# Kernel tuning notes

Measured on AMD Instinct MI355X. Metric: run time of the kernel, lower is better.

## Reference

```python
import jax, jax.numpy as jnp
import numpy as np

N = 4096        # nodes == batch_size (GFN operates on dense N x N adjacency)
E = 65536       # edges per view (avg degree 16)
IN = 512        # per-view input feature dim
HV = [128, 64]  # per-view GCN dims
HM = [64, 64]   # fused-graph GCN dims
VIEWS = 3


def setup_inputs() -> dict:
    key = jax.random.key(0)
    ks = iter(jax.random.split(key, 64))

    def xavier(shape):
        lim = float(np.sqrt(6.0 / (shape[0] + shape[1])))
        return jax.random.uniform(next(ks), shape, minval=-lim, maxval=lim, dtype=jnp.float32)

    inp = {}
    for v in range(VIEWS):
        inp[f"x{v}"] = jax.random.normal(next(ks), (N, IN), dtype=jnp.float32)
        inp[f"src{v}"] = jax.random.randint(next(ks), (E,), 0, N, dtype=jnp.int32)
        inp[f"dst{v}"] = jax.random.randint(next(ks), (E,), 0, N, dtype=jnp.int32)
        inp[f"Wv{v}0"] = xavier((IN, HV[0]))
        inp[f"bv{v}0"] = jnp.zeros((HV[0],), jnp.float32)
        inp[f"Wv{v}1"] = xavier((HV[0], HV[1]))
        inp[f"bv{v}1"] = jnp.zeros((HV[1],), jnp.float32)
        inp[f"Wf{v}"] = xavier((HV[1], HV[1]))  # FeatureFusion weight
    # GFN: Linear(N -> N/2) -> ReLU -> Linear(N/2 -> N)
    inp["Wg1"] = xavier((N, N // 2)); inp["bg1"] = jnp.zeros((N // 2,), jnp.float32)
    inp["Wg2"] = xavier((N // 2, N)); inp["bg2"] = jnp.zeros((N,), jnp.float32)
    # fused-graph GCN layers
    inp["Wm0"] = xavier((HV[1], HM[0])); inp["bm0"] = jnp.zeros((HM[0],), jnp.float32)
    inp["Wm1"] = xavier((HM[0], HM[1])); inp["bm1"] = jnp.zeros((HM[1],), jnp.float32)
    return inp


def _deg_norms(src, dst):
    # DGL GraphConv norm='both': scale by out-deg(src)^-1/2 and in-deg(dst)^-1/2, degrees clamped to >=1
    ones = jnp.ones(src.shape[0], jnp.float32)
    dout = jnp.maximum(jax.ops.segment_sum(ones, src, num_segments=N), 1.0)
    din = jnp.maximum(jax.ops.segment_sum(ones, dst, num_segments=N), 1.0)
    return dout ** -0.5, din ** -0.5


def _gconv(x, W, b, src, dst, do_isqrt, di_isqrt, act):
    h = (x * do_isqrt[:, None]) @ W            # [N, out] (W commutes with row scaling)
    agg = jax.ops.segment_sum(h[src], dst, num_segments=N)
    h = agg * di_isqrt[:, None] + b
    return act(h)


def reference(x0, x1, x2, src0, dst0, src1, dst1, src2, dst2,
              Wv00, bv00, Wv01, bv01, Wv10, bv10, Wv11, bv11, Wv20, bv20, Wv21, bv21,
              Wf0, Wf1, Wf2, Wg1, bg1, Wg2, bg2, Wm0, bm0, Wm1, bm1):
    ident = lambda t: t
    xs = [x0, x1, x2]
    edges = [(src0, dst0), (src1, dst1), (src2, dst2)]
    Wv = [(Wv00, bv00, Wv01, bv01), (Wv10, bv10, Wv11, bv11), (Wv20, bv20, Wv21, bv21)]
    Wf = [Wf0, Wf1, Wf2]

    # per-view GCN stacks (relu on first layer, identity on last)
    feats = []
    for v in range(VIEWS):
        src, dst = edges[v]
        do_i, di_i = _deg_norms(src, dst)
        W0, b0, W1, b1 = Wv[v]
        f = _gconv(xs[v], W0, b0, src, dst, do_i, di_i, jax.nn.relu)
        f = _gconv(f, W1, b1, src, dst, do_i, di_i, ident)
        feats.append(f)

    # FeatureFusion (dropout omitted for determinism): sum(f @ Wf), softmax over features, relu
    z = feats[0] @ Wf[0] + feats[1] @ Wf[1] + feats[2] @ Wf[2]
    z = jax.nn.relu(jax.nn.softmax(z, axis=1))

    # consensus graph: sum of per-view dense adjacencies -> GFN -> clamp -> round(+0.1)
    adj = jnp.zeros((N, N), jnp.float32)
    for src, dst in edges:
        adj = adj + jnp.zeros((N, N), jnp.float32).at[src, dst].set(1.0)
    fused = jax.nn.relu(adj @ Wg1 + bg1) @ Wg2 + bg2
    fused = jnp.round(jnp.clip(fused, 0.0, 1.0) + 0.1)
    adj_r = fused

    # rebuild binary graph (went through numpy in original -> stop_gradient), symmetrize, add self-loops
    sym = jax.lax.stop_gradient(fused)
    sym = sym + sym.T
    A = jnp.maximum((sym > 0).astype(jnp.float32), jnp.eye(N, dtype=jnp.float32))
    deg = A.sum(axis=1)
    dn = deg ** -0.5

    # fused-graph GCN layers (dense normalized SpMM form since A is already dense)
    h = z
    h = jax.nn.relu(((A @ (h * dn[:, None])) * dn[:, None]) @ Wm0 + bm0)
    h = ((A @ (h * dn[:, None])) * dn[:, None]) @ Wm1 + bm1

    # InnerProductDecoder with identity activation; all `views` entries of adj_rec are identical
    adj_rec = h @ h.T
    return (adj_r, adj_rec, h)
```

## Files before the change

kernel.cpp:

```cpp
#include <hip/hip_runtime.h>
#include <math.h>

#define NNODES 4096
#define NEDGES 65536

typedef short bf16x8 __attribute__((ext_vector_type(8)));
typedef short short4v __attribute__((ext_vector_type(4)));
typedef float f32x4 __attribute__((ext_vector_type(4)));

struct Ptr3  { const float* p[3]; };
struct Ptr3i { const int*   p[3]; };
struct Ptr3h { const short* p[3]; };

__device__ __forceinline__ short f2bf(float f) {
    unsigned u = __builtin_bit_cast(unsigned, f);
    unsigned r = (u + 0x7FFFu + ((u >> 16) & 1u)) >> 16;
    return (short)r;
}

__device__ __forceinline__ void gload_lds16(const void* g, void* l) {
    __builtin_amdgcn_global_load_lds(
        (const __attribute__((address_space(1))) unsigned*)g,
        (__attribute__((address_space(3))) unsigned*)l, 16, 0, 0);
}

template<int ACT>
__global__ __launch_bounds__(512, 1)
void g8_k(const short* __restrict__ A, const short* __restrict__ Bt,
          const float* __restrict__ bias, void* __restrict__ Cout,
          unsigned char* __restrict__ Pout, int M, int Nn, int K, int lda, int ldb)
{
    constexpr int SLOT = 24576;
    __shared__ short lds[3 * SLOT];
    const int tid = threadIdx.x;
    const int lane = tid & 63;
    const int wave = tid >> 6;
    const int wm = wave >> 1, wn = wave & 1;
    const int gx = gridDim.x, nwg = gx * gridDim.y;
    int w = blockIdx.y * gx + blockIdx.x;
    const int q8 = nwg >> 3;
    w = (w & 7) * q8 + (w >> 3);
    const int bm0 = (w / gx) * 256, bn0 = (w % gx) * 128;
    const int NT = K >> 6;

    auto stageR = [&](int t, int part) {
        if (t >= NT) return;
        const int k0 = t << 6;
        char* base = (char*)(lds + (t % 3) * SLOT);
#pragma unroll
        for (int r = 0; r < 2; ++r) {
            int ra = part * 2 + r;
            int o = ra * 8192 + tid * 16;
            int row = o >> 7;
            int sl = (o >> 4) & 7;
            gload_lds16(A + ((size_t)(bm0 + row) * lda + k0 + ((sl ^ (row & 7)) << 3)),
                        base + ra * 8192 + wave * 1024);
        }
        {
            int o = part * 8192 + tid * 16;
            int row = o >> 7;
            int sl = (o >> 4) & 7;
            gload_lds16(Bt + ((size_t)(bn0 + row) * ldb + k0 + ((sl ^ (row & 7)) << 3)),
                        base + 32768 + part * 8192 + wave * 1024);
        }
    };

    f32x4 acc[4][4] = {};
    bf16x8 bF[4][2];

    stageR(0, 0); stageR(0, 1);
    stageR(1, 0); stageR(1, 1);
    asm volatile("s_waitcnt vmcnt(6)" ::: "memory");
    __builtin_amdgcn_sched_barrier(0);
    __builtin_amdgcn_s_barrier();

    for (int t = 0; t < NT; ++t) {
        const short* As_ = lds + (t % 3) * SLOT;
        const short* Bs_ = As_ + 16384;
        bf16x8 aF[2][2];
#pragma unroll
        for (int kk = 0; kk < 2; ++kk) {
            const int h = kk * 4 + (lane >> 4);
#pragma unroll
            for (int j = 0; j < 4; ++j) {
                int r = wn * 64 + j * 16 + (lane & 15);
                bF[j][kk] = *(const bf16x8*)(Bs_ + r * 64 + ((h ^ (r & 7)) << 3));
            }
#pragma unroll
            for (int i = 0; i < 2; ++i) {
                int r = wm * 64 + i * 16 + (lane & 15);
                aF[i][kk] = *(const bf16x8*)(As_ + r * 64 + ((h ^ (r & 7)) << 3));
            }
        }
        stageR(t + 2, 0);
        __builtin_amdgcn_s_barrier();
        __builtin_amdgcn_s_setprio(1);
#pragma unroll
        for (int kk = 0; kk < 2; ++kk)
#pragma unroll
            for (int i = 0; i < 2; ++i)
#pragma unroll
                for (int j = 0; j < 4; ++j)
                    acc[i][j] = __builtin_amdgcn_mfma_f32_16x16x32_bf16(
                        aF[i][kk], bF[j][kk], acc[i][j], 0, 0, 0);
        __builtin_amdgcn_s_setprio(0);
        __builtin_amdgcn_s_barrier();
#pragma unroll
        for (int kk = 0; kk < 2; ++kk) {
            const int h = kk * 4 + (lane >> 4);
#pragma unroll
            for (int i = 0; i < 2; ++i) {
                int r = wm * 64 + 32 + i * 16 + (lane & 15);
                aF[i][kk] = *(const bf16x8*)(As_ + r * 64 + ((h ^ (r & 7)) << 3));
            }
        }
        stageR(t + 2, 1);
        __builtin_amdgcn_s_barrier();
        __builtin_amdgcn_s_setprio(1);
#pragma unroll
        for (int kk = 0; kk < 2; ++kk)
#pragma unroll
            for (int i = 0; i < 2; ++i)
#pragma unroll
                for (int j = 0; j < 4; ++j)
                    acc[2 + i][j] = __builtin_amdgcn_mfma_f32_16x16x32_bf16(
                        aF[i][kk], bF[j][kk], acc[2 + i][j], 0, 0, 0);
        __builtin_amdgcn_s_setprio(0);
        if (t + 2 < NT) { asm volatile("s_waitcnt vmcnt(6)" ::: "memory"); }
        else            { asm volatile("s_waitcnt vmcnt(0)" ::: "memory"); }
        __builtin_amdgcn_sched_barrier(0);
        __builtin_amdgcn_s_barrier();
    }

    const int cr = (lane >> 4) * 4;
    const int cc = lane & 15;
#pragma unroll
    for (int im = 0; im < 4; ++im) {
#pragma unroll
        for (int j = 0; j < 4; ++j) {
            int col = bn0 + wn * 64 + j * 16 + cc;
            float bv = bias ? bias[col] : 0.f;
#pragma unroll
            for (int q2 = 0; q2 < 4; ++q2) {
                int row = bm0 + wm * 64 + (im >> 1) * 32 + (im & 1) * 16 + cr + q2;
                float v = acc[im][j][q2] + bv;
                if constexpr (ACT == 1) {
                    v = fmaxf(v, 0.f);
                    ((short*)Cout)[(size_t)row * Nn + col] = f2bf(v);
                } else if constexpr (ACT == 2) {
                    v = rintf(fminf(fmaxf(v, 0.f), 1.f) + 0.1f);
                    ((float*)Cout)[(size_t)row * Nn + col] = v;
                    Pout[(size_t)row * Nn + col] = (unsigned char)(v > 0.5f);
                } else {
                    ((float*)Cout)[(size_t)row * Nn + col] = v;
                }
            }
        }
    }
}

__global__ __launch_bounds__(256)
void mfma_gemm_b_k(const short* __restrict__ Aall, Ptr3h Btv, float* __restrict__ Call,
                   int M, int Nn, int K)
{
    __shared__ short As[64 * 64];
    __shared__ short Bs[64 * 64];
    const int z = blockIdx.z;
    const short* A = Aall + (size_t)z * M * K;
    const short* Bt = Btv.p[z];
    float* C = Call + (size_t)z * M * Nn;
    const int tid = threadIdx.x;
    const int lane = tid & 63, wave = tid >> 6;
    const int bm0 = blockIdx.y * 64, bn0 = blockIdx.x * 64;
    const int wr = (wave >> 1) * 32, wc = (wave & 1) * 32;

    f32x4 acc[2][2] = {};

    for (int k0 = 0; k0 < K; k0 += 64) {
        for (int c = wave; c < 8; c += 4) {
            int o = c * 1024 + lane * 16;
            int row = o >> 7;
            int sl = (o >> 4) & 7;
            int ss = sl ^ (row & 7);
            gload_lds16(A + ((size_t)(bm0 + row) * K + k0 + ss * 8), As + c * 512);
            gload_lds16(Bt + ((size_t)(bn0 + row) * K + k0 + ss * 8), Bs + c * 512);
        }
        __syncthreads();
#pragma unroll
        for (int kk = 0; kk < 2; ++kk) {
            bf16x8 a[2], b[2];
            const int khalf = kk * 4 + (lane >> 4);
#pragma unroll
            for (int i = 0; i < 2; ++i) {
                int r = wr + i * 16 + (lane & 15);
                a[i] = *(const bf16x8*)(As + r * 64 + ((khalf ^ (r & 7)) << 3));
            }
#pragma unroll
            for (int j = 0; j < 2; ++j) {
                int r = wc + j * 16 + (lane & 15);
                b[j] = *(const bf16x8*)(Bs + r * 64 + ((khalf ^ (r & 7)) << 3));
            }
#pragma unroll
            for (int i = 0; i < 2; ++i)
#pragma unroll
                for (int j = 0; j < 2; ++j)
                    acc[i][j] = __builtin_amdgcn_mfma_f32_16x16x32_bf16(a[i], b[j], acc[i][j], 0, 0, 0);
        }
        __syncthreads();
    }

    const int cr = (lane >> 4) * 4;
    const int cc = lane & 15;
#pragma unroll
    for (int i = 0; i < 2; ++i)
#pragma unroll
        for (int j = 0; j < 2; ++j)
#pragma unroll
            for (int q = 0; q < 4; ++q) {
                int row = bm0 + wr + i * 16 + cr + q;
                int col = bn0 + wc + j * 16 + cc;
                C[(size_t)row * Nn + col] = acc[i][j][q];
            }
}

__global__ __launch_bounds__(256)
void spmm_mfma_k(const short* __restrict__ A2b, const short* __restrict__ XsT,
                 float* __restrict__ part)
{
    __shared__ short As[64 * 64];
    __shared__ short Bs[128 * 64];
    const int tid = threadIdx.x;
    const int lane = tid & 63, wave = tid >> 6;
    const int kc = blockIdx.x, m0 = blockIdx.y * 64;
    const int wr = (wave >> 1) * 32, wc = (wave & 1) * 32;
    const int woff = wave * 512;

    f32x4 acc[2][2] = {};

    for (int k0 = kc * 512; k0 < kc * 512 + 512; k0 += 64) {
#pragma unroll
        for (int r = 0; r < 2; ++r) {
            int o = r * 4096 + tid * 16;
            int row = o >> 7;
            int sl = (o >> 4) & 7;
            gload_lds16(A2b + ((size_t)(m0 + row) * 4096 + k0 + ((sl ^ (row & 7)) << 3)),
                        As + r * 2048 + woff);
        }
#pragma unroll
        for (int r = 0; r < 4; ++r) {
            int o = r * 4096 + tid * 16;
            int row = o >> 7;
            int sl = (o >> 4) & 7;
            gload_lds16(XsT + ((size_t)row * 4096 + k0 + ((sl ^ (row & 7)) << 3)),
                        Bs + r * 2048 + woff);
        }
        __syncthreads();
#pragma unroll
        for (int kk = 0; kk < 2; ++kk) {
            const int h = kk * 4 + (lane >> 4);
            bf16x8 a[2], bh[2], bl[2];
#pragma unroll
            for (int i = 0; i < 2; ++i) {
                int r = wr + i * 16 + (lane & 15);
                a[i] = *(const bf16x8*)(As + r * 64 + ((h ^ (r & 7)) << 3));
            }
#pragma unroll
            for (int j = 0; j < 2; ++j) {
                int r = wc + j * 16 + (lane & 15);
                bh[j] = *(const bf16x8*)(Bs + r * 64 + ((h ^ (r & 7)) << 3));
                int r2 = r + 64;
                bl[j] = *(const bf16x8*)(Bs + r2 * 64 + ((h ^ (r2 & 7)) << 3));
            }
#pragma unroll
            for (int i = 0; i < 2; ++i)
#pragma unroll
                for (int j = 0; j < 2; ++j) {
                    acc[i][j] = __builtin_amdgcn_mfma_f32_16x16x32_bf16(a[i], bh[j], acc[i][j], 0, 0, 0);
                    acc[i][j] = __builtin_amdgcn_mfma_f32_16x16x32_bf16(a[i], bl[j], acc[i][j], 0, 0, 0);
                }
        }
        __syncthreads();
    }

    const int cr = (lane >> 4) * 4;
    const int cc = lane & 15;
#pragma unroll
    for (int i = 0; i < 2; ++i)
#pragma unroll
        for (int j = 0; j < 2; ++j)
#pragma unroll
            for (int q = 0; q < 4; ++q)
                part[((size_t)kc * NNODES + m0 + wr + i * 16 + cr + q) * 64 + wc + j * 16 + cc]
                    = acc[i][j][q];
}

__global__ void xsT_k(const float* __restrict__ X, const int* __restrict__ degA,
                      short* __restrict__ XsT)
{
    const int n = blockIdx.y;
    const int k = blockIdx.x * 256 + threadIdx.x;
    float v = X[(size_t)k * 64 + n] * (1.0f / sqrtf((float)degA[k]));
    short hi = f2bf(v);
    float hif = __builtin_bit_cast(float, ((unsigned)(unsigned short)hi) << 16);
    short lo = f2bf(v - hif);
    XsT[(size_t)n * 4096 + k] = hi;
    XsT[(size_t)(64 + n) * 4096 + k] = lo;
}

__global__ void a2b_k(const unsigned* __restrict__ A8w, short* __restrict__ A2b, int words)
{
    int t = blockIdx.x * 256 + threadIdx.x;
    if (t < words) {
        unsigned w = A8w[t];
        short4v o;
#pragma unroll
        for (int j = 0; j < 4; ++j) o[j] = ((w >> (8 * j)) & 1u) ? (short)0x3F80 : (short)0;
        *(short4v*)(A2b + (size_t)t * 4) = o;
    }
}

__global__ void f32_to_bf16T_k(const float* __restrict__ src, short* __restrict__ dstT,
                               int R, int C)
{
    __shared__ float t[64][65];
    const int br = blockIdx.y * 64, bc = blockIdx.x * 64;
    for (int idx = threadIdx.x; idx < 64 * 64; idx += 256) {
        int r = idx >> 6, c = idx & 63;
        t[r][c] = src[(size_t)(br + r) * C + bc + c];
    }
    __syncthreads();
    for (int idx = threadIdx.x; idx < 64 * 64; idx += 256) {
        int c = idx >> 6, r = idx & 63;
        dstT[(size_t)(bc + c) * R + br + r] = f2bf(t[r][c]);
    }
}

__global__ void mask_to_bf16_k(const unsigned* __restrict__ mask, short* __restrict__ adj,
                               int words)
{
    int t = blockIdx.x * 256 + threadIdx.x;
    if (t < words) {
        unsigned w = mask[t];
        short4v o;
        o.x = f2bf((float)__popc(w & 0x7u));
        o.y = f2bf((float)__popc(w & 0x700u));
        o.z = f2bf((float)__popc(w & 0x70000u));
        o.w = f2bf((float)__popc(w & 0x7000000u));
        *(short4v*)(adj + (size_t)t * 4) = o;
    }
}

__global__ void xsplit_k(Ptr3 xv, const float* __restrict__ isq, short* __restrict__ xe)
{
    const int z = blockIdx.y;
    int t = blockIdx.x * 256 + threadIdx.x;
    int n = t >> 9, k = t & 511;
    float a = xv.p[z][(size_t)n * 512 + k] * isq[2 * z * NNODES + n];
    short hi = f2bf(a);
    float hif = __builtin_bit_cast(float, ((unsigned)(unsigned short)hi) << 16);
    short lo = f2bf(a - hif);
    short* row = xe + (size_t)z * NNODES * 1536 + (size_t)n * 1536;
    row[k] = hi; row[512 + k] = hi; row[1024 + k] = lo;
}

__global__ void wsplitT_k(Ptr3 Wv, short* __restrict__ out, int K, int Nn)
{
    const int z = blockIdx.y;
    int t = blockIdx.x * 256 + threadIdx.x;
    if (t >= K * Nn) return;
    int k = t / Nn, n = t % Nn;
    float w = Wv.p[z][(size_t)k * Nn + n];
    short hi = f2bf(w);
    float hif = __builtin_bit_cast(float, ((unsigned)(unsigned short)hi) << 16);
    short lo = f2bf(w - hif);
    short* row = out + (size_t)z * Nn * 3 * K + (size_t)n * 3 * K;
    row[k] = hi; row[K + k] = lo; row[2 * K + k] = hi;
}

template<int RELU>
__global__ __launch_bounds__(256)
void redgemm_k(const float* __restrict__ part, const int* __restrict__ degA,
               const float* __restrict__ Wm, const float* __restrict__ bias,
               float* __restrict__ out, short* __restrict__ Ae, short* __restrict__ Be)
{
    __shared__ float Ws[64 * 64];
    const int tid = threadIdx.x;
    for (int i = tid; i < 4096; i += 256) Ws[i] = Wm[i];
    __syncthreads();
    const int lane = tid & 63, wave = tid >> 6;
    const float bv = bias[lane];
    for (int rr = 0; rr < 4; ++rr) {
        int row = blockIdx.x * 16 + wave * 4 + rr;
        float s = 0.f;
#pragma unroll
        for (int p = 0; p < 8; ++p) s += part[((size_t)p * NNODES + row) * 64 + lane];
        s *= 1.0f / sqrtf((float)degA[row]);
        float acc = bv;
#pragma unroll
        for (int k = 0; k < 64; ++k)
            acc = fmaf(__shfl(s, k), Ws[k * 64 + lane], acc);
        if (RELU) acc = fmaxf(acc, 0.f);
        out[(size_t)row * 64 + lane] = acc;
        if (Ae) {
            short hi = f2bf(acc);
            float hif = __builtin_bit_cast(float, ((unsigned)(unsigned short)hi) << 16);
            short lo = f2bf(acc - hif);
            size_t ro = (size_t)row * 192;
            Ae[ro + lane] = hi; Ae[ro + 64 + lane] = hi; Ae[ro + 128 + lane] = lo;
            Be[ro + lane] = hi; Be[ro + 64 + lane] = lo; Be[ro + 128 + lane] = hi;
        }
    }
}

__global__ void edge_k(Ptr3i src, Ptr3i dst, unsigned* __restrict__ mask, int* __restrict__ degs)
{
    int e = blockIdx.x * 256 + threadIdx.x;
    int z = blockIdx.y;
    if (e < NEDGES) {
        int s = src.p[z][e], d = dst.p[z][e];
        unsigned c = (unsigned)s * (unsigned)NNODES + (unsigned)d;
        atomicOr(&mask[c >> 2], 1u << ((c & 3u) * 8u + (unsigned)z));
        atomicAdd(&degs[2 * z * NNODES + s], 1);
        atomicAdd(&degs[(2 * z + 1) * NNODES + d], 1);
    }
}

__global__ void deg_norm_k(const int* __restrict__ degs, float* __restrict__ isq, int n)
{
    int t = blockIdx.x * 256 + threadIdx.x;
    if (t < n) isq[t] = 1.0f / sqrtf(fmaxf((float)degs[t], 1.0f));
}

__global__ __launch_bounds__(1024)
void scan_k(const int* __restrict__ degs, int* __restrict__ rowptr, int* __restrict__ cursor)
{
    const int z = blockIdx.x;
    const int* din = degs + (2 * z + 1) * NNODES;
    __shared__ int sm[1024];
    const int t = threadIdx.x;
    int v0 = din[t * 4], v1 = din[t * 4 + 1], v2 = din[t * 4 + 2], v3 = din[t * 4 + 3];
    int c1 = v0 + v1, c2 = c1 + v2, s = c2 + v3;
    sm[t] = s;
    __syncthreads();
    for (int off = 1; off < 1024; off <<= 1) {
        int add = (t >= off) ? sm[t - off] : 0;
        __syncthreads();
        sm[t] += add;
        __syncthreads();
    }
    int base = sm[t] - s;
    int* rp = rowptr + z * NNODES;
    int* cu = cursor + z * NNODES;
    rp[t * 4] = base;          cu[t * 4] = base;
    rp[t * 4 + 1] = base + v0; cu[t * 4 + 1] = base + v0;
    rp[t * 4 + 2] = base + c1; cu[t * 4 + 2] = base + c1;
    rp[t * 4 + 3] = base + c2; cu[t * 4 + 3] = base + c2;
}

__global__ void fill_k(Ptr3i src, Ptr3i dst, int* __restrict__ cursor, int* __restrict__ eidx)
{
    int e = blockIdx.x * 256 + threadIdx.x;
    int z = blockIdx.y;
    if (e < NEDGES) {
        int d = dst.p[z][e];
        int pos = atomicAdd(&cursor[z * NNODES + d], 1);
        eidx[(size_t)z * NEDGES + pos] = src.p[z][e];
    }
}

template<int F, int ACT, int MODE>
__global__ void gather_k(const float* __restrict__ Hpre, const int* __restrict__ eidx,
                         const int* __restrict__ rowptr, const int* __restrict__ degs,
                         const float* __restrict__ isq, Ptr3 bias, short* __restrict__ Sout)
{
    const int z = blockIdx.y;
    const int tid = threadIdx.x;
    const int node = blockIdx.x * (256 / F) + tid / F;
    const int f = tid % F;
    const float* H = Hpre + (size_t)z * NNODES * F;
    const int base = rowptr[z * NNODES + node];
    const int cnt = degs[(2 * z + 1) * NNODES + node];
    const int* ei = eidx + (size_t)z * NEDGES + base;
    float s = 0.f;
    for (int i = 0; i < cnt; ++i) s += H[(size_t)ei[i] * F + f];
    float v = s * isq[(2 * z + 1) * NNODES + node] + bias.p[z][f];
    if (ACT) v = fmaxf(v, 0.f);
    if (MODE == 1) v *= isq[2 * z * NNODES + node];
    short hi = f2bf(v);
    float hif = __builtin_bit_cast(float, ((unsigned)(unsigned short)hi) << 16);
    short lo = f2bf(v - hif);
    short* row = Sout + (size_t)z * NNODES * 3 * F + (size_t)node * 3 * F;
    row[f] = hi; row[F + f] = hi; row[2 * F + f] = lo;
}

__global__ void softsum_k(const float* __restrict__ zp, float* __restrict__ z)
{
    int row = blockIdx.x * 4 + (threadIdx.x >> 6);
    int f = threadIdx.x & 63;
    size_t i = (size_t)row * 64 + f;
    float v = zp[i] + zp[i + (size_t)NNODES * 64] + zp[i + (size_t)2 * NNODES * 64];
    float m = v;
#pragma unroll
    for (int off = 32; off >= 1; off >>= 1) m = fmaxf(m, __shfl_xor(m, off));
    float e = expf(v - m);
    float s = e;
#pragma unroll
    for (int off = 32; off >= 1; off >>= 1) s += __shfl_xor(s, off);
    z[i] = e / s;
}

__global__ __launch_bounds__(256)
void build_A2_k(const unsigned char* __restrict__ P, unsigned char* __restrict__ A8,
                int* __restrict__ degA)
{
    __shared__ unsigned Ts[64][20];
    const int bi = blockIdx.y * 64, bj = blockIdx.x * 64;
    const int tid = threadIdx.x;
    const int r = tid >> 2, seg = tid & 3;
    uint4 tv = *(const uint4*)(P + (size_t)(bj + r) * NNODES + bi + seg * 16);
    Ts[r][seg * 4 + 0] = tv.x; Ts[r][seg * 4 + 1] = tv.y;
    Ts[r][seg * 4 + 2] = tv.z; Ts[r][seg * 4 + 3] = tv.w;
    __syncthreads();
    uint4 dv = *(const uint4*)(P + (size_t)(bi + r) * NNODES + bj + seg * 16);
    unsigned dw[4] = {dv.x, dv.y, dv.z, dv.w};
    const unsigned char* Tb = (const unsigned char*)Ts;
    unsigned ow[4];
    int psum = 0;
#pragma unroll
    for (int w = 0; w < 4; ++w) {
        unsigned o = 0;
#pragma unroll
        for (int b = 0; b < 4; ++b) {
            int j = seg * 16 + w * 4 + b;
            unsigned a = (dw[w] >> (8 * b)) & 1u;
            unsigned tr = Tb[j * 80 + r] & 1u;
            unsigned on = a | tr | (unsigned)((bi + r) == (bj + j));
            o |= on << (8 * b);
            psum += (int)on;
        }
        ow[w] = o;
    }
    uint4 o4; o4.x = ow[0]; o4.y = ow[1]; o4.z = ow[2]; o4.w = ow[3];
    *(uint4*)(A8 + (size_t)(bi + r) * NNODES + bj + seg * 16) = o4;
    psum += __shfl_xor(psum, 1);
    psum += __shfl_xor(psum, 2);
    if (seg == 0) atomicAdd(&degA[bi + r], psum);
}

extern "C" void kernel_launch(void* const* d_in, const int* in_sizes, int n_in,
                              void* d_out, int out_size, void* d_ws, size_t ws_size,
                              hipStream_t stream)
{
    const int N = NNODES, E = NEDGES;
    const size_t MB = 1024 * 1024;

    const float* x[3]; const int* src[3]; const int* dst[3];
    const float *Wv0[3], *bv0[3], *Wv1[3], *bv1[3], *Wf[3];
    for (int v = 0; v < 3; ++v) {
        const int b = v * 8;
        x[v]   = (const float*)d_in[b + 0];
        src[v] = (const int*)  d_in[b + 1];
        dst[v] = (const int*)  d_in[b + 2];
        Wv0[v] = (const float*)d_in[b + 3];
        bv0[v] = (const float*)d_in[b + 4];
        Wv1[v] = (const float*)d_in[b + 5];
        bv1[v] = (const float*)d_in[b + 6];
        Wf[v]  = (const float*)d_in[b + 7];
    }
    const float* Wg1 = (const float*)d_in[24];
    const float* bg1 = (const float*)d_in[25];
    const float* Wg2 = (const float*)d_in[26];
    const float* bg2 = (const float*)d_in[27];
    const float* Wm0 = (const float*)d_in[28];
    const float* bm0 = (const float*)d_in[29];
    const float* Wm1 = (const float*)d_in[30];
    const float* bm1 = (const float*)d_in[31];

    float* out_adjr = (float*)d_out;
    float* out_rec  = out_adjr + (size_t)N * N;
    float* out_h    = out_rec + (size_t)N * N;

    char* oa = (char*)out_adjr;
    short* AdjB = (short*)oa;
    float* hv1  = (float*)(oa + 32 * MB);
    short* Ae2  = (short*)(oa + 38 * MB);
    short* Ae3  = (short*)(oa + 47 * MB);
    float* hv2  = (float*)(oa + 52 * MB);
    float* zp   = (float*)(oa + 56 * MB);

    char* orc = (char*)out_rec;
    short* xe   = (short*)orc;
    short* H1b  = (short*)orc;
    unsigned char* P = (unsigned char*)(orc + 16 * MB);
    short* Wg1T = (short*)(orc + 16 * MB);
    short* Wg2T = (short*)(orc + 32 * MB);
    short* A2b  = (short*)orc;
    float* part = (float*)(orc + 48 * MB);

    char* p = (char*)d_ws;
    unsigned* mask = (unsigned*)p;
    unsigned char* A8 = (unsigned char*)p;
    short* AeF = (short*)p;
    short* BeF = AeF + (size_t)N * 192;
    p += (size_t)N * N;
    int* degs = (int*)p;     p += (size_t)6 * N * 4;
    float* isq = (float*)p;  p += (size_t)6 * N * 4;
    int* rowptr = (int*)p;   p += (size_t)3 * N * 4;
    int* cursor = (int*)p;   p += (size_t)3 * N * 4;
    int* eidx = (int*)p;     p += (size_t)3 * E * 4;
    int* degA = (int*)p;     p += (size_t)N * 4;
    float* zbuf = (float*)p; p += (size_t)N * 64 * 4;
    float* h1m = (float*)p;  p += (size_t)N * 64 * 4;
    short* XsT = (short*)p;  p += (size_t)128 * N * 2;
    short* Wv0T = (short*)p; p += (size_t)3 * 128 * 1536 * 2;
    short* Wv1T = (short*)p; p += (size_t)3 * 64 * 384 * 2;
    short* WfT  = (short*)p; p += (size_t)3 * 64 * 192 * 2;

    Ptr3i srcP, dstP;
    for (int v = 0; v < 3; ++v) { srcP.p[v] = src[v]; dstP.p[v] = dst[v]; }

    hipMemsetAsync(mask, 0, (size_t)N * N, stream);
    hipMemsetAsync(degs, 0, (size_t)6 * N * 4, stream);

    edge_k<<<dim3((E + 255) / 256, 3), 256, 0, stream>>>(srcP, dstP, mask, degs);
    deg_norm_k<<<(6 * N + 255) / 256, 256, 0, stream>>>(degs, isq, 6 * N);
    scan_k<<<3, 1024, 0, stream>>>(degs, rowptr, cursor);
    fill_k<<<dim3((E + 255) / 256, 3), 256, 0, stream>>>(srcP, dstP, cursor, eidx);

    Ptr3 xP; for (int v = 0; v < 3; ++v) xP.p[v] = x[v];
    xsplit_k<<<dim3(N * 512 / 256, 3), 256, 0, stream>>>(xP, isq, xe);
    Ptr3 wP;
    for (int v = 0; v < 3; ++v) wP.p[v] = Wv0[v];
    wsplitT_k<<<dim3(512 * 128 / 256, 3), 256, 0, stream>>>(wP, Wv0T, 512, 128);
    for (int v = 0; v < 3; ++v) wP.p[v] = Wv1[v];
    wsplitT_k<<<dim3(128 * 64 / 256, 3), 256, 0, stream>>>(wP, Wv1T, 128, 64);
    for (int v = 0; v < 3; ++v) wP.p[v] = Wf[v];
    wsplitT_k<<<dim3(64 * 64 / 256, 3), 256, 0, stream>>>(wP, WfT, 64, 64);

    Ptr3h BtP; Ptr3 biasP;
    for (int v = 0; v < 3; ++v) BtP.p[v] = Wv0T + (size_t)v * 128 * 1536;
    mfma_gemm_b_k<<<dim3(2, N / 64, 3), 256, 0, stream>>>(xe, BtP, hv1, N, 128, 1536);
    for (int v = 0; v < 3; ++v) biasP.p[v] = bv0[v];
    gather_k<128, 1, 1><<<dim3(N / 2, 3), 256, 0, stream>>>(hv1, eidx, rowptr, degs, isq, biasP, Ae2);
    for (int v = 0; v < 3; ++v) BtP.p[v] = Wv1T + (size_t)v * 64 * 384;
    mfma_gemm_b_k<<<dim3(1, N / 64, 3), 256, 0, stream>>>(Ae2, BtP, hv2, N, 64, 384);
    for (int v = 0; v < 3; ++v) biasP.p[v] = bv1[v];
    gather_k<64, 0, 2><<<dim3(N / 4, 3), 256, 0, stream>>>(hv2, eidx, rowptr, degs, isq, biasP, Ae3);
    for (int v = 0; v < 3; ++v) BtP.p[v] = WfT + (size_t)v * 64 * 192;
    mfma_gemm_b_k<<<dim3(1, N / 64, 3), 256, 0, stream>>>(Ae3, BtP, zp, N, 64, 192);
    softsum_k<<<N / 4, 256, 0, stream>>>(zp, zbuf);

    mask_to_bf16_k<<<(N * N / 4 + 255) / 256, 256, 0, stream>>>(mask, AdjB, N * N / 4);
    f32_to_bf16T_k<<<dim3(2048 / 64, 4096 / 64), 256, 0, stream>>>(Wg1, Wg1T, 4096, 2048);

    g8_k<1><<<dim3(2048 / 128, 4096 / 256), 512, 0, stream>>>(
        AdjB, Wg1T, bg1, H1b, nullptr, 4096, 2048, 4096, 4096, 4096);

    f32_to_bf16T_k<<<dim3(4096 / 64, 2048 / 64), 256, 0, stream>>>(Wg2, Wg2T, 2048, 4096);

    g8_k<2><<<dim3(4096 / 128, 4096 / 256), 512, 0, stream>>>(
        H1b, Wg2T, bg2, out_adjr, P, 4096, 4096, 2048, 2048, 2048);

    hipMemsetAsync(degA, 0, (size_t)N * 4, stream);
    build_A2_k<<<dim3(N / 64, N / 64), 256, 0, stream>>>(P, A8, degA);

    a2b_k<<<(N * N / 4 + 255) / 256, 256, 0, stream>>>((const unsigned*)A8, A2b, N * N / 4);
    xsT_k<<<dim3(16, 64), 256, 0, stream>>>(zbuf, degA, XsT);
    spmm_mfma_k<<<dim3(8, N / 64), 256, 0, stream>>>(A2b, XsT, part);
    redgemm_k<1><<<256, 256, 0, stream>>>(part, degA, Wm0, bm0, h1m, nullptr, nullptr);
    xsT_k<<<dim3(16, 64), 256, 0, stream>>>(h1m, degA, XsT);
    spmm_mfma_k<<<dim3(8, N / 64), 256, 0, stream>>>(A2b, XsT, part);
    redgemm_k<0><<<256, 256, 0, stream>>>(part, degA, Wm1, bm1, out_h, AeF, BeF);

    g8_k<0><<<dim3(4096 / 128, 4096 / 256), 512, 0, stream>>>(
        AeF, BeF, nullptr, out_rec, nullptr, 4096, 4096, 192, 192, 192);
}
```

Before: 455.1 us.

## Enlarge GEMM tiles to 256x256 and split-K the first GFN GEMM

Replaces the 256x128-tile GEMM with a 256x256-tile variant using 8 waves in a 2x4 grid and a double-buffered LDS with a quarter-phase schedule interleaving loads and MFMAs. The first GFN GEMM (4096x2048, K=4096) is split into two K halves via blockIdx.z writing fp32 partials, then summed with bias and ReLU into bf16 by a separate reduce kernel. This aims to raise arithmetic intensity per workgroup and keep enough workgroups in flight despite larger tiles. It adds extra fp32 partial traffic and a launch, and the larger tiles use more registers and LDS.

```diff
diff --git a/kernel.cpp b/kernel.cpp
--- a/kernel.cpp
+++ b/kernel.cpp
@@ -7,6 +7,7 @@
 typedef short bf16x8 __attribute__((ext_vector_type(8)));
 typedef short short4v __attribute__((ext_vector_type(4)));
 typedef float f32x4 __attribute__((ext_vector_type(4)));
+typedef float f32x4v __attribute__((ext_vector_type(4)));
 
 struct Ptr3  { const float* p[3]; };
 struct Ptr3i { const int*   p[3]; };
@@ -26,137 +27,157 @@
 
 template<int ACT>
 __global__ __launch_bounds__(512, 1)
-void g8_k(const short* __restrict__ A, const short* __restrict__ Bt,
-          const float* __restrict__ bias, void* __restrict__ Cout,
+void gm_k(const short* __restrict__ A, const short* __restrict__ Bt,
+          const float* __restrict__ bias, void* __restrict__ Cout, float* __restrict__ Cout1,
           unsigned char* __restrict__ Pout, int M, int Nn, int K, int lda, int ldb)
 {
-    constexpr int SLOT = 24576;
-    __shared__ short lds[3 * SLOT];
+    constexpr int SLOT = 32768;
+    __shared__ short lds[2 * SLOT];
     const int tid = threadIdx.x;
     const int lane = tid & 63;
     const int wave = tid >> 6;
-    const int wm = wave >> 1, wn = wave & 1;
+    const int wm = wave >> 2, wn = wave & 3;
+    const int z = blockIdx.z;
+    A  += (size_t)z * K;
+    Bt += (size_t)z * K;
+    float* Cf = (ACT == 3 && z == 1) ? Cout1 : (float*)Cout;
     const int gx = gridDim.x, nwg = gx * gridDim.y;
     int w = blockIdx.y * gx + blockIdx.x;
     const int q8 = nwg >> 3;
     w = (w & 7) * q8 + (w >> 3);
-    const int bm0 = (w / gx) * 256, bn0 = (w % gx) * 128;
+    const int bm0 = (w / gx) * 256, bn0 = (w % gx) * 256;
     const int NT = K >> 6;
 
-    auto stageR = [&](int t, int part) {
+    auto stageH = [&](int t, int part) {
         if (t >= NT) return;
         const int k0 = t << 6;
-        char* base = (char*)(lds + (t % 3) * SLOT);
+        char* base = (char*)(lds + (t & 1) * SLOT);
+        const int isB = (part < 2);
+        const int h = part & 1;
 #pragma unroll
         for (int r = 0; r < 2; ++r) {
-            int ra = part * 2 + r;
-            int o = ra * 8192 + tid * 16;
+            int o = r * 8192 + tid * 16;
             int row = o >> 7;
-            int sl = (o >> 4) & 7;
-            gload_lds16(A + ((size_t)(bm0 + row) * lda + k0 + ((sl ^ (row & 7)) << 3)),
-                        base + ra * 8192 + wave * 1024);
-        }
-        {
-            int o = part * 8192 + tid * 16;
-            int row = o >> 7;
-            int sl = (o >> 4) & 7;
-            gload_lds16(Bt + ((size_t)(bn0 + row) * ldb + k0 + ((sl ^ (row & 7)) << 3)),
-                        base + 32768 + part * 8192 + wave * 1024);
+            int grow = h * 128 + row;
+            int scol = (((o >> 4) & 7) ^ (grow & 7)) << 3;
+            const short* gsrc = isB ? (Bt + (size_t)(bn0 + grow) * ldb + k0 + scol)
+                                    : (A  + (size_t)(bm0 + grow) * lda + k0 + scol);
+            gload_lds16(gsrc, base + (isB ? 32768 : 0) + h * 16384 + r * 8192 + wave * 1024);
         }
     };
 
-    f32x4 acc[4][4] = {};
+    f32x4 acc[8][4] = {};
+    bf16x8 aF[4][2];
     bf16x8 bF[4][2];
 
-    stageR(0, 0); stageR(0, 1);
-    stageR(1, 0); stageR(1, 1);
-    asm volatile("s_waitcnt vmcnt(6)" ::: "memory");
+#define PH(QM, QN, TCUR, T1, P1, T2, P2, VM)                                          \
+    {                                                                                 \
+        const short* As_ = lds + ((TCUR) & 1) * SLOT;                                 \
+        const short* Bs_ = As_ + 16384;                                               \
+        if constexpr ((QN) == 0) {                                                    \
+            _Pragma("unroll") for (int kk = 0; kk < 2; ++kk) {                        \
+                const int h_ = kk * 4 + (lane >> 4);                                  \
+                _Pragma("unroll") for (int i = 0; i < 4; ++i) {                       \
+                    int r_ = wm * 128 + (QM) * 64 + i * 16 + (lane & 15);             \
+                    aF[i][kk] = *(const bf16x8*)(As_ + r_ * 64 + ((h_ ^ (r_ & 7)) << 3)); \
+                }                                                                     \
+            }                                                                         \
+        }                                                                             \
+        if constexpr ((QM) == 0) {                                                    \
+            _Pragma("unroll") for (int kk = 0; kk < 2; ++kk) {                        \
+                const int h_ = kk * 4 + (lane >> 4);                                  \
+                _Pragma("unroll") for (int j = 0; j < 2; ++j) {                       \
+                    int r_ = wn * 64 + ((QN) * 2 + j) * 16 + (lane & 15);             \
+                    bF[(QN) * 2 + j][kk] = *(const bf16x8*)(Bs_ + r_ * 64 + ((h_ ^ (r_ & 7)) << 3)); \
+                }                                                                     \
+            }                                                                         \
+        }                                                                             \
+        if ((P1) >= 0) stageH(T1, P1);                                                \
+        if ((P2) >= 0) stageH(T2, P2);                                                \
+        __builtin_amdgcn_s_barrier();                                                 \
+        __builtin_amdgcn_s_setprio(1);                                                \
+        _Pragma("unroll") for (int kk = 0; kk < 2; ++kk)                              \
+            _Pragma("unroll") for (int i = 0; i < 4; ++i)                             \
+                _Pragma("unroll") for (int j = 0; j < 2; ++j)                         \
+                    acc[(QM) * 4 + i][(QN) * 2 + j] =                                 \
+                        __builtin_amdgcn_mfma_f32_16x16x32_bf16(                      \
+                            aF[i][kk], bF[(QN) * 2 + j][kk],                          \
+                            acc[(QM) * 4 + i][(QN) * 2 + j], 0, 0, 0);                \
+        __builtin_amdgcn_s_setprio(0);                                                \
+        if ((VM) == 6)      { asm volatile("s_waitcnt vmcnt(6)" ::: "memory");        \
+                              __builtin_amdgcn_sched_barrier(0); }                    \
+        else if ((VM) == 0) { asm volatile("s_waitcnt vmcnt(0)" ::: "memory");        \
+                              __builtin_amdgcn_sched_barrier(0); }                    \
+        __builtin_amdgcn_s_barrier();                                                 \
+    }
+
+    stageH(0, 0); stageH(0, 1); stageH(0, 2); stageH(0, 3);
+    if (NT > 1) { stageH(1, 0); stageH(1, 1); stageH(1, 2); }
+    if (NT > 1) { asm volatile("s_waitcnt vmcnt(6)" ::: "memory"); }
+    else        { asm volatile("s_waitcnt vmcnt(0)" ::: "memory"); }
     __builtin_amdgcn_sched_barrier(0);
     __builtin_amdgcn_s_barrier();
 
-    for (int t = 0; t < NT; ++t) {
-        const short* As_ = lds + (t % 3) * SLOT;
-        const short* Bs_ = As_ + 16384;
-        bf16x8 aF[2][2];
-#pragma unroll
-        for (int kk = 0; kk < 2; ++kk) {
-            const int h = kk * 4 + (lane >> 4);
-#pragma unroll
-            for (int j = 0; j < 4; ++j) {
-                int r = wn * 64 + j * 16 + (lane & 15);
-                bF[j][kk] = *(const bf16x8*)(Bs_ + r * 64 + ((h ^ (r & 7)) << 3));
-            }
-#pragma unroll
-            for (int i = 0; i < 2; ++i) {
-                int r = wm * 64 + i * 16 + (lane & 15);
-                aF[i][kk] = *(const bf16x8*)(As_ + r * 64 + ((h ^ (r & 7)) << 3));
-            }
-        }
-        stageR(t + 2, 0);
-        __builtin_amdgcn_s_barrier();
-        __builtin_amdgcn_s_setprio(1);
-#pragma unroll
-        for (int kk = 0; kk < 2; ++kk)
-#pragma unroll
-            for (int i = 0; i < 2; ++i)
-#pragma unroll
-                for (int j = 0; j < 4; ++j)
-                    acc[i][j] = __builtin_amdgcn_mfma_f32_16x16x32_bf16(
-                        aF[i][kk], bF[j][kk], acc[i][j], 0, 0, 0);
-        __builtin_amdgcn_s_setprio(0);
-        __builtin_amdgcn_s_barrier();
-#pragma unroll
-        for (int kk = 0; kk < 2; ++kk) {
-            const int h = kk * 4 + (lane >> 4);
-#pragma unroll
-            for (int i = 0; i < 2; ++i) {
-                int r = wm * 64 + 32 + i * 16 + (lane & 15);
-                aF[i][kk] = *(const bf16x8*)(As_ + r * 64 + ((h ^ (r & 7)) << 3));
-            }
-        }
-        stageR(t + 2, 1);
-        __builtin_amdgcn_s_barrier();
-        __builtin_amdgcn_s_setprio(1);
-#pragma unroll
-        for (int kk = 0; kk < 2; ++kk)
-#pragma unroll
-            for (int i = 0; i < 2; ++i)
-#pragma unroll
-                for (int j = 0; j < 4; ++j)
-                    acc[2 + i][j] = __builtin_amdgcn_mfma_f32_16x16x32_bf16(
-                        aF[i][kk], bF[j][kk], acc[2 + i][j], 0, 0, 0);
-        __builtin_amdgcn_s_setprio(0);
-        if (t + 2 < NT) { asm volatile("s_waitcnt vmcnt(6)" ::: "memory"); }
-        else            { asm volatile("s_waitcnt vmcnt(0)" ::: "memory"); }
-        __builtin_amdgcn_sched_barrier(0);
-        __builtin_amdgcn_s_barrier();
-    }
+    for (int it = 0; it < NT / 2; ++it) {
+        const int t0 = 2 * it, t1 = t0 + 1, t2 = t0 + 2, t3 = t0 + 3;
+        const int vm4 = (t2 < NT) ? 6 : 0;
+        const int vm8 = (t3 < NT) ? 6 : 0;
+        PH(0, 0, t0, t1, 3,  0, -1, -1)
+        PH(0, 1, t0,  0, -1, 0, -1, -1)
+        PH(1, 0, t0, t2, 0, t2,  1, -1)
+        PH(1, 1, t0, t2, 2,  0, -1, vm4)
+        PH(0, 0, t1, t2, 3,  0, -1, -1)
+        PH(0, 1, t1,  0, -1, 0, -1, -1)
+        PH(1, 0, t1, t3, 0, t3,  1, -1)
+        PH(1, 1, t1, t3, 2,  0, -1, vm8)
+    }
+    if (NT & 1) {
+        const int tl = NT - 1;
+        PH(0, 0, tl, 0, -1, 0, -1, -1)
+        PH(0, 1, tl, 0, -1, 0, -1, -1)
+        PH(1, 0, tl, 0, -1, 0, -1, -1)
+        PH(1, 1, tl, 0, -1, 0, -1, -1)
+    }
+#undef PH
 
     const int cr = (lane >> 4) * 4;
     const int cc = lane & 15;
 #pragma unroll
-    for (int im = 0; im < 4; ++im) {
-#pragma unroll
-        for (int j = 0; j < 4; ++j) {
-            int col = bn0 + wn * 64 + j * 16 + cc;
+    for (int im = 0; im < 8; ++im) {
+#pragma unroll
+        for (int jn = 0; jn < 4; ++jn) {
+            int col = bn0 + wn * 64 + jn * 16 + cc;
             float bv = bias ? bias[col] : 0.f;
 #pragma unroll
             for (int q2 = 0; q2 < 4; ++q2) {
-                int row = bm0 + wm * 64 + (im >> 1) * 32 + (im & 1) * 16 + cr + q2;
-                float v = acc[im][j][q2] + bv;
-                if constexpr (ACT == 1) {
-                    v = fmaxf(v, 0.f);
-                    ((short*)Cout)[(size_t)row * Nn + col] = f2bf(v);
-                } else if constexpr (ACT == 2) {
+                int row = bm0 + wm * 128 + (im >> 2) * 64 + (im & 3) * 16 + cr + q2;
+                float v = acc[im][jn][q2] + bv;
+                if constexpr (ACT == 2) {
                     v = rintf(fminf(fmaxf(v, 0.f), 1.f) + 0.1f);
-                    ((float*)Cout)[(size_t)row * Nn + col] = v;
+                    Cf[(size_t)row * Nn + col] = v;
                     Pout[(size_t)row * Nn + col] = (unsigned char)(v > 0.5f);
                 } else {
-                    ((float*)Cout)[(size_t)row * Nn + col] = v;
+                    Cf[(size_t)row * Nn + col] = v;
                 }
             }
         }
     }
+}
+
+__global__ void reduce_h1_k(const float* __restrict__ p0, const float* __restrict__ p1,
+                            const float* __restrict__ bias, short* __restrict__ H1b)
+{
+    int i = (blockIdx.x * 256 + threadIdx.x) * 4;
+    f32x4v a = *(const f32x4v*)(p0 + i);
+    f32x4v b = *(const f32x4v*)(p1 + i);
+    int col = i & 2047;
+    short4v o;
+#pragma unroll
+    for (int j = 0; j < 4; ++j) {
+        float v = a[j] + b[j] + bias[col + j];
+        o[j] = f2bf(fmaxf(v, 0.f));
+    }
+    *(short4v*)(H1b + i) = o;
 }
 
 __global__ __launch_bounds__(256)
@@ -587,12 +608,14 @@
     short* Ae3  = (short*)(oa + 47 * MB);
     float* hv2  = (float*)(oa + 52 * MB);
     float* zp   = (float*)(oa + 56 * MB);
+    float* partg0 = (float*)(oa + 32 * MB);
 
     char* orc = (char*)out_rec;
     short* xe   = (short*)orc;
     short* H1b  = (short*)orc;
     unsigned char* P = (unsigned char*)(orc + 16 * MB);
     short* Wg1T = (short*)(orc + 16 * MB);
+    float* partg1 = (float*)(orc + 32 * MB);
     short* Wg2T = (short*)(orc + 32 * MB);
     short* A2b  = (short*)orc;
     float* part = (float*)(orc + 48 * MB);
@@ -653,13 +676,14 @@
     mask_to_bf16_k<<<(N * N / 4 + 255) / 256, 256, 0, stream>>>(mask, AdjB, N * N / 4);
     f32_to_bf16T_k<<<dim3(2048 / 64, 4096 / 64), 256, 0, stream>>>(Wg1, Wg1T, 4096, 2048);
 
-    g8_k<1><<<dim3(2048 / 128, 4096 / 256), 512, 0, stream>>>(
-        AdjB, Wg1T, bg1, H1b, nullptr, 4096, 2048, 4096, 4096, 4096);
+    gm_k<3><<<dim3(2048 / 256, 4096 / 256, 2), 512, 0, stream>>>(
+        AdjB, Wg1T, nullptr, partg0, partg1, nullptr, 4096, 2048, 2048, 4096, 4096);
+    reduce_h1_k<<<4096 * 2048 / 4 / 256, 256, 0, stream>>>(partg0, partg1, bg1, H1b);
 
     f32_to_bf16T_k<<<dim3(4096 / 64, 2048 / 64), 256, 0, stream>>>(Wg2, Wg2T, 2048, 4096);
 
-    g8_k<2><<<dim3(4096 / 128, 4096 / 256), 512, 0, stream>>>(
-        H1b, Wg2T, bg2, out_adjr, P, 4096, 4096, 2048, 2048, 2048);
+    gm_k<2><<<dim3(4096 / 256, 4096 / 256, 1), 512, 0, stream>>>(
+        H1b, Wg2T, bg2, out_adjr, nullptr, P, 4096, 4096, 2048, 2048, 2048);
 
     hipMemsetAsync(degA, 0, (size_t)N * 4, stream);
     build_A2_k<<<dim3(N / 64, N / 64), 256, 0, stream>>>(P, A8, degA);
@@ -672,6 +696,6 @@
     spmm_mfma_k<<<dim3(8, N / 64), 256, 0, stream>>>(A2b, XsT, part);
     redgemm_k<0><<<256, 256, 0, stream>>>(part, degA, Wm1, bm1, out_h, AeF, BeF);
 
-    g8_k<0><<<dim3(4096 / 128, 4096 / 256), 512, 0, stream>>>(
-        AeF, BeF, nullptr, out_rec, nullptr, 4096, 4096, 192, 192, 192);
-}
+    gm_k<0><<<dim3(4096 / 256, 4096 / 256, 1), 512, 0, stream>>>(
+        AeF, BeF, nullptr, out_rec, nullptr, nullptr, 4096, 4096, 192, 192, 192);
+}
```

Measured after the change: 452.8 us. Within noise of the previous version (-0.5%).
